# Kernel tuning notes

Hardware: AMD Instinct MI355X
Metric: run time of the kernel (lower is better)

The kernel has to match this reference:

```python
import jax, jax.numpy as jnp
import numpy as np

CHEB_K = 3


def cheb_gcn(x, node_emb, w_pool, b_pool):
    # x: [B, N, C], node_emb: [N, D], w_pool: [D, K, C, O], b_pool: [D, O]
    n = node_emb.shape[0]
    A = jax.nn.softmax(jax.nn.relu(node_emb @ node_emb.T), axis=1)  # [N, N]
    supports = [jnp.eye(n, dtype=x.dtype), A]
    for _ in range(2, CHEB_K):
        supports.append(2.0 * A @ supports[-1] - supports[-2])
    S = jnp.stack(supports, axis=0)  # [K, N, N]
    weights = jnp.einsum('nd,dkio->nkio', node_emb, w_pool)  # [N, K, C, O]
    bias = node_emb @ b_pool  # [N, O]
    x_g = jnp.einsum('knm,bmc->bnkc', S, x)  # [B, N, K, C]
    return jnp.einsum('bnki,nkio->bno', x_g, weights) + bias


def setup_inputs() -> dict:
    key = jax.random.key(0)
    ks = jax.random.split(key, 7)
    B, N, DIN, DOUT, E = 64, 1024, 64, 64, 16
    C = DIN + DOUT
    return {
        'x': jax.random.normal(ks[0], (B, N, DIN), jnp.float32),
        'state': jax.random.normal(ks[1], (B, N, DOUT), jnp.float32),
        'node_embeddings': jax.random.normal(ks[2], (N, E), jnp.float32),
        'W_gate': jax.random.normal(ks[3], (E, CHEB_K, C, 2 * DOUT), jnp.float32) * 0.1,
        'b_gate': jax.random.normal(ks[4], (E, 2 * DOUT), jnp.float32) * 0.1,
        'W_update': jax.random.normal(ks[5], (E, CHEB_K, C, DOUT), jnp.float32) * 0.1,
        'b_update': jax.random.normal(ks[6], (E, DOUT), jnp.float32) * 0.1,
    }


def reference(x, state, node_embeddings, W_gate, b_gate, W_update, b_update):
    hidden = state.shape[-1]
    inp = jnp.concatenate([x, state], axis=-1)  # [B, N, DIN+DOUT]
    z_r = jax.nn.sigmoid(cheb_gcn(inp, node_embeddings, W_gate, b_gate))
    z, r = z_r[..., :hidden], z_r[..., hidden:]
    cand = jnp.concatenate([x, r * state], axis=-1)
    h_hat = jnp.tanh(cheb_gcn(cand, node_embeddings, W_update, b_update))
    return z * state + (1.0 - z) * h_hat
```

## Files before the change

### kernel.cpp

```cpp
#include <hip/hip_runtime.h>
#include <hip/hip_bf16.h>
#include <math.h>

#define B_ 64
#define N_ 1024
#define E_ 16

typedef unsigned short ushort_t;
typedef __attribute__((ext_vector_type(8))) short bf16x8;
typedef __attribute__((ext_vector_type(4))) float f32x4;

__device__ __forceinline__ float sigmoidf_(float x) {
  return 1.0f / (1.0f + __expf(-x));
}
__device__ __forceinline__ ushort_t f2bf(float f) {
  unsigned int u = __float_as_uint(f);
  u = (u + 0x7fffu + ((u >> 16) & 1u)) >> 16;
  return (ushort_t)u;
}
__device__ __forceinline__ float bf2f(ushort_t h) { return __uint_as_float((unsigned)h << 16); }
__device__ __forceinline__ void split_bf(float x, ushort_t& h, ushort_t& l) {
  h = f2bf(x);
  l = f2bf(x - bf2f(h));
}
__device__ __forceinline__ void gload16(const void* g, void* l) {
  __builtin_amdgcn_global_load_lds(
      (const __attribute__((address_space(1))) unsigned int*)g,
      (__attribute__((address_space(3))) unsigned int*)l, 16, 0, 0);
}

__global__ __launch_bounds__(256) void compute_A_kernel(const float* __restrict__ emb,
                                                        ushort_t* __restrict__ Ah,
                                                        ushort_t* __restrict__ Al) {
  __shared__ float embn[E_];
  __shared__ float red[256];
  const int n = blockIdx.x;
  const int t = threadIdx.x;
  if (t < E_) embn[t] = emb[n * E_ + t];
  __syncthreads();
  float s[4];
#pragma unroll
  for (int j = 0; j < 4; ++j) {
    const int m = j * 256 + t;
    const float* em = emb + m * E_;
    float acc = 0.f;
#pragma unroll
    for (int d = 0; d < E_; ++d) acc = fmaf(embn[d], em[d], acc);
    s[j] = fmaxf(acc, 0.f);
  }
  float mx = fmaxf(fmaxf(s[0], s[1]), fmaxf(s[2], s[3]));
  red[t] = mx;
  __syncthreads();
  for (int off = 128; off > 0; off >>= 1) {
    if (t < off) red[t] = fmaxf(red[t], red[t + off]);
    __syncthreads();
  }
  mx = red[0];
  __syncthreads();
  float e[4], lsum = 0.f;
#pragma unroll
  for (int j = 0; j < 4; ++j) { e[j] = __expf(s[j] - mx); lsum += e[j]; }
  red[t] = lsum;
  __syncthreads();
  for (int off = 128; off > 0; off >>= 1) {
    if (t < off) red[t] += red[t + off];
    __syncthreads();
  }
  const float inv = 1.0f / red[0];
#pragma unroll
  for (int j = 0; j < 4; ++j) {
    const float v = e[j] * inv;
    ushort_t h, l;
    split_bf(v, h, l);
    Ah[n * N_ + j * 256 + t] = h;
    Al[n * N_ + j * 256 + t] = l;
  }
}

__global__ __launch_bounds__(256) void build_T0t_kernel(const float* __restrict__ xA,
                                                        const float* __restrict__ xB,
                                                        ushort_t* __restrict__ Th,
                                                        ushort_t* __restrict__ Tl) {
  __shared__ float tile[128][129];
  const int t = threadIdx.x;
  const int b = blockIdx.y;
  const int n0 = blockIdx.x << 7;
  const int c4 = (t & 31) << 2, nl = t >> 5;
#pragma unroll
  for (int p = 0; p < 16; ++p) {
    const int n = nl + (p << 3);
    const float4 v = (c4 < 64)
        ? *(const float4*)&xA[((size_t)b << 16) + ((size_t)(n0 + n) << 6) + c4]
        : *(const float4*)&xB[((size_t)b << 16) + ((size_t)(n0 + n) << 6) + c4 - 64];
    tile[c4 + 0][n] = v.x; tile[c4 + 1][n] = v.y;
    tile[c4 + 2][n] = v.z; tile[c4 + 3][n] = v.w;
  }
  __syncthreads();
  const int c = t >> 1, nc = (t & 1) << 6;
  const size_t obase = ((size_t)(b << 7) + c) * 1024 + n0 + nc;
#pragma unroll
  for (int u = 0; u < 64; u += 4) {
    ushort4 h, l;
    split_bf(tile[c][nc + u + 0], h.x, l.x);
    split_bf(tile[c][nc + u + 1], h.y, l.y);
    split_bf(tile[c][nc + u + 2], h.z, l.z);
    split_bf(tile[c][nc + u + 3], h.w, l.w);
    *(ushort4*)&Th[obase + u] = h;
    *(ushort4*)&Tl[obase + u] = l;
  }
}

template <int PHASE>
__global__ __launch_bounds__(256, 2) void mfma_gemm_kernel(
    const ushort_t* __restrict__ Ah, const ushort_t* __restrict__ Al,
    const ushort_t* __restrict__ Bh, const ushort_t* __restrict__ Bl,
    const ushort_t* __restrict__ T0th, const ushort_t* __restrict__ T0tl,
    float* __restrict__ Yf, ushort_t* __restrict__ Yth, ushort_t* __restrict__ Ytl) {
  __shared__ ushort_t Ah_s[128 * 64], Al_s[128 * 64], Bh_s[128 * 64], Bl_s[128 * 64];
  const int t = threadIdx.x;
  const int wave = t >> 6, lane = t & 63;
  const int n0 = blockIdx.y << 7;
  const int j0 = blockIdx.x << 7;
  const int wr = wave >> 1, wc = wave & 1;
  const int fr = lane & 15, fk = lane >> 4;

  f32x4 acc[4][4];
#pragma unroll
  for (int i = 0; i < 4; ++i)
#pragma unroll
    for (int j = 0; j < 4; ++j) acc[i][j] = (f32x4){0.f, 0.f, 0.f, 0.f};

  const int rsub = lane >> 3;
  const int cp = lane & 7;
  const int selem = (((cp << 4) ^ (rsub << 4)) >> 1);

  for (int k0 = 0; k0 < 1024; k0 += 64) {
    __syncthreads();
#pragma unroll
    for (int i = 0; i < 4; ++i) {
      const int q = (wave << 2) + i;
      const int row = (q << 3) + rsub;
      const int lo = (q << 9) + lane * 8;
      const size_t ga = (size_t)(n0 + row) * 1024 + k0 + selem;
      const size_t gb = (size_t)(j0 + row) * 1024 + k0 + selem;
      gload16(Ah + ga, Ah_s + lo);
      gload16(Al + ga, Al_s + lo);
      gload16(Bh + gb, Bh_s + lo);
      gload16(Bl + gb, Bl_s + lo);
    }
    __syncthreads();
#pragma unroll
    for (int ks = 0; ks < 2; ++ks) {
      bf16x8 ah[4], al[4], bh[4], bl[4];
#pragma unroll
      for (int mi = 0; mi < 4; ++mi) {
        const int r = (wr << 6) + (mi << 4) + fr;
        const int kb = ((ks << 6) + (fk << 4)) ^ ((r & 7) << 4);
        ah[mi] = *(const bf16x8*)((const char*)Ah_s + r * 128 + kb);
        al[mi] = *(const bf16x8*)((const char*)Al_s + r * 128 + kb);
      }
#pragma unroll
      for (int nj = 0; nj < 4; ++nj) {
        const int r = (wc << 6) + (nj << 4) + fr;
        const int kb = ((ks << 6) + (fk << 4)) ^ ((r & 7) << 4);
        bh[nj] = *(const bf16x8*)((const char*)Bh_s + r * 128 + kb);
        bl[nj] = *(const bf16x8*)((const char*)Bl_s + r * 128 + kb);
      }
#pragma unroll
      for (int mi = 0; mi < 4; ++mi)
#pragma unroll
        for (int nj = 0; nj < 4; ++nj) {
          acc[mi][nj] = __builtin_amdgcn_mfma_f32_16x16x32_bf16(ah[mi], bh[nj], acc[mi][nj], 0, 0, 0);
          acc[mi][nj] = __builtin_amdgcn_mfma_f32_16x16x32_bf16(ah[mi], bl[nj], acc[mi][nj], 0, 0, 0);
          acc[mi][nj] = __builtin_amdgcn_mfma_f32_16x16x32_bf16(al[mi], bh[nj], acc[mi][nj], 0, 0, 0);
        }
    }
  }

#pragma unroll
  for (int mi = 0; mi < 4; ++mi) {
    const int nb = n0 + (wr << 6) + (mi << 4) + (fk << 2);
#pragma unroll
    for (int nj = 0; nj < 4; ++nj) {
      const int j = j0 + (wc << 6) + (nj << 4) + fr;
      const f32x4 v = acc[mi][nj];
      if (PHASE == 1) {
#pragma unroll
        for (int r = 0; r < 4; ++r) Yf[(size_t)(nb + r) * 8192 + j] = v[r];
        ushort4 h, l;
        split_bf(v[0], h.x, l.x); split_bf(v[1], h.y, l.y);
        split_bf(v[2], h.z, l.z); split_bf(v[3], h.w, l.w);
        *(ushort4*)&Yth[(size_t)j * 1024 + nb] = h;
        *(ushort4*)&Ytl[(size_t)j * 1024 + nb] = l;
      } else {
        const ushort4 th = *(const ushort4*)&T0th[(size_t)j * 1024 + nb];
        const ushort4 tl = *(const ushort4*)&T0tl[(size_t)j * 1024 + nb];
        float t0r[4];
        t0r[0] = bf2f(th.x) + bf2f(tl.x); t0r[1] = bf2f(th.y) + bf2f(tl.y);
        t0r[2] = bf2f(th.z) + bf2f(tl.z); t0r[3] = bf2f(th.w) + bf2f(tl.w);
#pragma unroll
        for (int r = 0; r < 4; ++r) Yf[(size_t)(nb + r) * 8192 + j] = 2.0f * v[r] - t0r[r];
      }
    }
  }
}

template <int OW_SRC>
__global__ __launch_bounds__(256) void wcombine_half_kernel(const float* __restrict__ emb,
                                                            const float* __restrict__ Wp,
                                                            int o0,
                                                            ushort_t* __restrict__ Wn) {
  __shared__ float es[8][E_];
  const int t = threadIdx.x;
  const int n0 = blockIdx.y * 8;
  if (t < 8 * E_) es[t >> 4][t & 15] = emb[n0 * E_ + t];
  __syncthreads();
  const int j = blockIdx.x * 1024 + t * 4;
  const int k = j >> 13, rem = j & 8191;
  const int i = rem >> 6, o = rem & 63;
  const size_t srcj = (size_t)(k * 128 + i) * OW_SRC + o0 + o;
  const size_t dstr = (size_t)3 * 128 * OW_SRC;
  float4 acc[8] = {};
#pragma unroll 4
  for (int d = 0; d < E_; ++d) {
    const float4 w = *(const float4*)&Wp[d * dstr + srcj];
#pragma unroll
    for (int g = 0; g < 8; ++g) {
      const float e = es[g][d];
      acc[g].x = fmaf(e, w.x, acc[g].x);
      acc[g].y = fmaf(e, w.y, acc[g].y);
      acc[g].z = fmaf(e, w.z, acc[g].z);
      acc[g].w = fmaf(e, w.w, acc[g].w);
    }
  }
#pragma unroll
  for (int g = 0; g < 8; ++g) {
    ushort4 o4;
    o4.x = f2bf(acc[g].x); o4.y = f2bf(acc[g].y);
    o4.z = f2bf(acc[g].z); o4.w = f2bf(acc[g].w);
    *(ushort4*)&Wn[(size_t)(n0 + g) * 24576 + j] = o4;
  }
}

template <int MODE>
__global__ __launch_bounds__(256) void pernode64_kernel(
    const float* __restrict__ xA, const float* __restrict__ xB,
    const float* __restrict__ Y1f, const float* __restrict__ Y2f,
    const ushort_t* __restrict__ Wn,
    const float* __restrict__ emb, const float* __restrict__ bsrc, int bstride,
    const float* __restrict__ state, const float* __restrict__ zb,
    float* __restrict__ dst) {
  __shared__ float XkT[128][68];
  __shared__ float Wf[64][64];
  __shared__ float embn[E_];
  __shared__ float bias[64];
  const int n = blockIdx.x;
  const int t = threadIdx.x;
  if (t < E_) embn[t] = emb[n * E_ + t];
  __syncthreads();
  if (t < 64) {
    float a = 0.f;
#pragma unroll
    for (int d = 0; d < E_; ++d) a = fmaf(embn[d], bsrc[d * bstride + t], a);
    bias[t] = a;
  }
  const int tx = t & 15, ty = t >> 4;
  float acc[4][4] = {};
  const ushort_t* Wb = Wn + (size_t)n * 24576;
#pragma unroll
  for (int k = 0; k < 3; ++k) {
    __syncthreads();
    {
      const int b = t & 63, i0 = (t >> 6) * 32;
      const float* src;
      if (k == 0)
        src = (i0 < 64) ? xA + ((size_t)b << 16) + ((size_t)n << 6) + i0
                        : xB + ((size_t)b << 16) + ((size_t)n << 6) + i0 - 64;
      else if (k == 1)
        src = Y1f + (size_t)n * 8192 + b * 128 + i0;
      else
        src = Y2f + (size_t)n * 8192 + b * 128 + i0;
#pragma unroll
      for (int i = 0; i < 32; ++i) XkT[i0 + i][b] = src[i];
    }
#pragma unroll
    for (int h = 0; h < 2; ++h) {
      if (h) __syncthreads();
      {
        const ushort_t* wsrc = Wb + k * 8192 + h * 4096;
#pragma unroll
        for (int r = 0; r < 2; ++r) {
          const int off = r * 2048 + t * 8;
          const uint4 p = *(const uint4*)&wsrc[off];
          float* dstp = &Wf[0][0] + off;
          dstp[0] = bf2f((ushort_t)(p.x & 0xffff)); dstp[1] = bf2f((ushort_t)(p.x >> 16));
          dstp[2] = bf2f((ushort_t)(p.y & 0xffff)); dstp[3] = bf2f((ushort_t)(p.y >> 16));
          dstp[4] = bf2f((ushort_t)(p.z & 0xffff)); dstp[5] = bf2f((ushort_t)(p.z >> 16));
          dstp[6] = bf2f((ushort_t)(p.w & 0xffff)); dstp[7] = bf2f((ushort_t)(p.w >> 16));
        }
      }
      __syncthreads();
      const int ib = h * 64;
#pragma unroll 4
      for (int ii = 0; ii < 64; ++ii) {
        float xv[4], w[4];
        *(float4*)&xv[0] = *(const float4*)&XkT[ib + ii][ty << 2];
        *(float4*)&w[0] = *(const float4*)&Wf[ii][tx << 2];
#pragma unroll
        for (int bi = 0; bi < 4; ++bi)
#pragma unroll
          for (int oj = 0; oj < 4; ++oj) acc[bi][oj] = fmaf(xv[bi], w[oj], acc[bi][oj]);
      }
    }
  }
#pragma unroll
  for (int bi = 0; bi < 4; ++bi) {
    const int b = (ty << 2) + bi;
    const size_t base = ((size_t)b << 16) + ((size_t)n << 6) + (tx << 2);
    float4 o;
    const float a0 = acc[bi][0] + bias[(tx << 2) + 0];
    const float a1 = acc[bi][1] + bias[(tx << 2) + 1];
    const float a2 = acc[bi][2] + bias[(tx << 2) + 2];
    const float a3 = acc[bi][3] + bias[(tx << 2) + 3];
    if (MODE == 0) {
      o.x = sigmoidf_(a0); o.y = sigmoidf_(a1); o.z = sigmoidf_(a2); o.w = sigmoidf_(a3);
    } else if (MODE == 1) {
      const float4 st = *(const float4*)&state[base];
      o.x = sigmoidf_(a0) * st.x; o.y = sigmoidf_(a1) * st.y;
      o.z = sigmoidf_(a2) * st.z; o.w = sigmoidf_(a3) * st.w;
    } else {
      const float4 st = *(const float4*)&state[base];
      const float4 zv = *(const float4*)&zb[base];
      o.x = zv.x * st.x + (1.f - zv.x) * tanhf(a0);
      o.y = zv.y * st.y + (1.f - zv.y) * tanhf(a1);
      o.z = zv.z * st.z + (1.f - zv.z) * tanhf(a2);
      o.w = zv.w * st.w + (1.f - zv.w) * tanhf(a3);
    }
    *(float4*)&dst[base] = o;
  }
}

extern "C" void kernel_launch(void* const* d_in, const int* in_sizes, int n_in,
                              void* d_out, int out_size, void* d_ws, size_t ws_size,
                              hipStream_t stream) {
  const float* x     = (const float*)d_in[0];
  const float* state = (const float*)d_in[1];
  const float* emb   = (const float*)d_in[2];
  const float* Wg    = (const float*)d_in[3];
  const float* bg    = (const float*)d_in[4];
  const float* Wu    = (const float*)d_in[5];
  const float* bu    = (const float*)d_in[6];
  float* out = (float*)d_out;

  char* w = (char*)d_ws;
  float*    Y1f  = (float*)(w);
  float*    Y2f  = (float*)(w + ((size_t)32 << 20));
  ushort_t* T0th = (ushort_t*)(w + ((size_t)64 << 20));
  ushort_t* T0tl = (ushort_t*)(w + ((size_t)80 << 20));
  ushort_t* Y1th = (ushort_t*)(w + ((size_t)96 << 20));
  ushort_t* Y1tl = (ushort_t*)(w + ((size_t)112 << 20));
  float*    rs   = (float*)(w + ((size_t)128 << 20));
  ushort_t* Ah   = (ushort_t*)(w + ((size_t)144 << 20));
  ushort_t* Al   = (ushort_t*)(w + ((size_t)146 << 20));
  ushort_t* Wn   = (ushort_t*)(w + ((size_t)148 << 20));
  float* zb = out;

  const dim3 gg(64, 8);
  const dim3 gt(8, 64);
  const dim3 gw(24, 128);

  compute_A_kernel<<<N_, 256, 0, stream>>>(emb, Ah, Al);

  build_T0t_kernel<<<gt, 256, 0, stream>>>(x, state, T0th, T0tl);
  mfma_gemm_kernel<1><<<gg, 256, 0, stream>>>(Ah, Al, T0th, T0tl, nullptr, nullptr, Y1f, Y1th, Y1tl);
  mfma_gemm_kernel<0><<<gg, 256, 0, stream>>>(Ah, Al, Y1th, Y1tl, T0th, T0tl, Y2f, nullptr, nullptr);
  wcombine_half_kernel<128><<<gw, 256, 0, stream>>>(emb, Wg, 0, Wn);
  pernode64_kernel<0><<<N_, 256, 0, stream>>>(x, state, Y1f, Y2f, Wn, emb, bg, 128,
                                              nullptr, nullptr, zb);
  wcombine_half_kernel<128><<<gw, 256, 0, stream>>>(emb, Wg, 64, Wn);
  pernode64_kernel<1><<<N_, 256, 0, stream>>>(x, state, Y1f, Y2f, Wn, emb, bg + 64, 128,
                                              state, nullptr, rs);

  build_T0t_kernel<<<gt, 256, 0, stream>>>(x, rs, T0th, T0tl);
  mfma_gemm_kernel<1><<<gg, 256, 0, stream>>>(Ah, Al, T0th, T0tl, nullptr, nullptr, Y1f, Y1th, Y1tl);
  mfma_gemm_kernel<0><<<gg, 256, 0, stream>>>(Ah, Al, Y1th, Y1tl, T0th, T0tl, Y2f, nullptr, nullptr);
  wcombine_half_kernel<64><<<gw, 256, 0, stream>>>(emb, Wu, 0, Wn);
  pernode64_kernel<2><<<N_, 256, 0, stream>>>(x, rs, Y1f, Y2f, Wn, emb, bu, 64,
                                              state, zb, out);
}
```

Measured before the change: 491.2 us.

## Fold T0 subtraction into weights and use MFMA for per-node contraction

The Chebyshev identity S2 = 2A^2 - I is applied by folding the -T0 term into the k=0 weights (W0 - W2). The second GEMM then just scales by 2 and no longer reads T0 in its epilogue. Both GEMMs now write split bf16 hi/lo node-major tiles through LDS instead of fp32 Y buffers. The per-node contraction is rewritten from scalar FP32 FMA to bf16x3 MFMA, with swizzled LDS and async global-to-LDS loads of the pre-transposed weights. This removes the scalar FMA bottleneck and halves the intermediate traffic, at the cost of bf16-split precision in the per-node stage.

```diff
diff --git a/kernel.cpp b/kernel.cpp
--- a/kernel.cpp
+++ b/kernel.cpp
@@ -19,10 +19,6 @@
   return (ushort_t)u;
 }
 __device__ __forceinline__ float bf2f(ushort_t h) { return __uint_as_float((unsigned)h << 16); }
-__device__ __forceinline__ void split_bf(float x, ushort_t& h, ushort_t& l) {
-  h = f2bf(x);
-  l = f2bf(x - bf2f(h));
-}
 __device__ __forceinline__ void gload16(const void* g, void* l) {
   __builtin_amdgcn_global_load_lds(
       (const __attribute__((address_space(1))) unsigned int*)g,
@@ -70,10 +66,9 @@
 #pragma unroll
   for (int j = 0; j < 4; ++j) {
     const float v = e[j] * inv;
-    ushort_t h, l;
-    split_bf(v, h, l);
+    ushort_t h = f2bf(v);
     Ah[n * N_ + j * 256 + t] = h;
-    Al[n * N_ + j * 256 + t] = l;
+    Al[n * N_ + j * 256 + t] = f2bf(v - bf2f(h));
   }
 }
 
@@ -101,10 +96,12 @@
 #pragma unroll
   for (int u = 0; u < 64; u += 4) {
     ushort4 h, l;
-    split_bf(tile[c][nc + u + 0], h.x, l.x);
-    split_bf(tile[c][nc + u + 1], h.y, l.y);
-    split_bf(tile[c][nc + u + 2], h.z, l.z);
-    split_bf(tile[c][nc + u + 3], h.w, l.w);
+    float v0 = tile[c][nc + u + 0], v1 = tile[c][nc + u + 1];
+    float v2 = tile[c][nc + u + 2], v3 = tile[c][nc + u + 3];
+    h.x = f2bf(v0); l.x = f2bf(v0 - bf2f(h.x));
+    h.y = f2bf(v1); l.y = f2bf(v1 - bf2f(h.y));
+    h.z = f2bf(v2); l.z = f2bf(v2 - bf2f(h.z));
+    h.w = f2bf(v3); l.w = f2bf(v3 - bf2f(h.w));
     *(ushort4*)&Th[obase + u] = h;
     *(ushort4*)&Tl[obase + u] = l;
   }
@@ -114,13 +111,18 @@
 __global__ __launch_bounds__(256, 2) void mfma_gemm_kernel(
     const ushort_t* __restrict__ Ah, const ushort_t* __restrict__ Al,
     const ushort_t* __restrict__ Bh, const ushort_t* __restrict__ Bl,
-    const ushort_t* __restrict__ T0th, const ushort_t* __restrict__ T0tl,
-    float* __restrict__ Yf, ushort_t* __restrict__ Yth, ushort_t* __restrict__ Ytl) {
-  __shared__ ushort_t Ah_s[128 * 64], Al_s[128 * 64], Bh_s[128 * 64], Bl_s[128 * 64];
+    ushort_t* __restrict__ Yth, ushort_t* __restrict__ Ytl,
+    ushort_t* __restrict__ XpH, ushort_t* __restrict__ XpL) {
+  __shared__ ushort_t smem[4 * 128 * 64];
+  ushort_t* Ah_s = smem;
+  ushort_t* Al_s = smem + 8192;
+  ushort_t* Bh_s = smem + 16384;
+  ushort_t* Bl_s = smem + 24576;
   const int t = threadIdx.x;
   const int wave = t >> 6, lane = t & 63;
   const int n0 = blockIdx.y << 7;
-  const int j0 = blockIdx.x << 7;
+  const int bcol = blockIdx.x;
+  const int j0 = bcol << 7;
   const int wr = wave >> 1, wc = wave & 1;
   const int fr = lane & 15, fk = lane >> 4;
 
@@ -177,53 +179,72 @@
     }
   }
 
+  __syncthreads();
+  ushort_t* hiT = smem;
+  ushort_t* loT = smem + 16384;
 #pragma unroll
   for (int mi = 0; mi < 4; ++mi) {
-    const int nb = n0 + (wr << 6) + (mi << 4) + (fk << 2);
+    const int nl = (wr << 6) + (mi << 4) + (fk << 2);
 #pragma unroll
     for (int nj = 0; nj < 4; ++nj) {
-      const int j = j0 + (wc << 6) + (nj << 4) + fr;
-      const f32x4 v = acc[mi][nj];
+      const int jl = (wc << 6) + (nj << 4) + fr;
+      const f32x4 vv = acc[mi][nj];
+      ushort_t h[4], l[4];
+#pragma unroll
+      for (int r = 0; r < 4; ++r) {
+        const float v = (PHASE == 1) ? vv[r] : 2.0f * vv[r];
+        h[r] = f2bf(v);
+        l[r] = f2bf(v - bf2f(h[r]));
+      }
       if (PHASE == 1) {
-#pragma unroll
-        for (int r = 0; r < 4; ++r) Yf[(size_t)(nb + r) * 8192 + j] = v[r];
-        ushort4 h, l;
-        split_bf(v[0], h.x, l.x); split_bf(v[1], h.y, l.y);
-        split_bf(v[2], h.z, l.z); split_bf(v[3], h.w, l.w);
-        *(ushort4*)&Yth[(size_t)j * 1024 + nb] = h;
-        *(ushort4*)&Ytl[(size_t)j * 1024 + nb] = l;
-      } else {
-        const ushort4 th = *(const ushort4*)&T0th[(size_t)j * 1024 + nb];
-        const ushort4 tl = *(const ushort4*)&T0tl[(size_t)j * 1024 + nb];
-        float t0r[4];
-        t0r[0] = bf2f(th.x) + bf2f(tl.x); t0r[1] = bf2f(th.y) + bf2f(tl.y);
-        t0r[2] = bf2f(th.z) + bf2f(tl.z); t0r[3] = bf2f(th.w) + bf2f(tl.w);
-#pragma unroll
-        for (int r = 0; r < 4; ++r) Yf[(size_t)(nb + r) * 8192 + j] = 2.0f * v[r] - t0r[r];
-      }
-    }
+        *(ushort4*)&Yth[(size_t)(j0 + jl) * 1024 + n0 + nl] = make_ushort4(h[0], h[1], h[2], h[3]);
+        *(ushort4*)&Ytl[(size_t)(j0 + jl) * 1024 + n0 + nl] = make_ushort4(l[0], l[1], l[2], l[3]);
+      }
+#pragma unroll
+      for (int r = 0; r < 4; ++r) {
+        hiT[(nl + r) * 128 + jl] = h[r];
+        loT[(nl + r) * 128 + jl] = l[r];
+      }
+    }
+  }
+  __syncthreads();
+#pragma unroll
+  for (int rr = 0; rr < 8; ++rr) {
+    const int id = rr * 256 + t;
+    const int nl = id >> 4, ch = id & 15;
+    const size_t dstE = ((size_t)(n0 + nl) * 64 + bcol) * 256 + ch * 8;
+    *(uint4*)&XpH[dstE] = *(const uint4*)((const char*)hiT + nl * 256 + ch * 16);
+    *(uint4*)&XpL[dstE] = *(const uint4*)((const char*)loT + nl * 256 + ch * 16);
   }
 }
 
 template <int OW_SRC>
-__global__ __launch_bounds__(256) void wcombine_half_kernel(const float* __restrict__ emb,
-                                                            const float* __restrict__ Wp,
-                                                            int o0,
-                                                            ushort_t* __restrict__ Wn) {
+__global__ __launch_bounds__(256) void wcombine_t_kernel(const float* __restrict__ emb,
+                                                         const float* __restrict__ Wp,
+                                                         int o0,
+                                                         ushort_t* __restrict__ WtH,
+                                                         ushort_t* __restrict__ WtL) {
   __shared__ float es[8][E_];
+  __shared__ ushort_t tileH[8][8][128];
+  __shared__ ushort_t tileL[8][8][128];
   const int t = threadIdx.x;
   const int n0 = blockIdx.y * 8;
+  const int k  = blockIdx.x >> 3;
+  const int ob = blockIdx.x & 7;
   if (t < 8 * E_) es[t >> 4][t & 15] = emb[n0 * E_ + t];
   __syncthreads();
-  const int j = blockIdx.x * 1024 + t * 4;
-  const int k = j >> 13, rem = j & 8191;
-  const int i = rem >> 6, o = rem & 63;
-  const size_t srcj = (size_t)(k * 128 + i) * OW_SRC + o0 + o;
-  const size_t dstr = (size_t)3 * 128 * OW_SRC;
+  const int i = t >> 1, oq = (t & 1) * 4;
+  const size_t dstr = (size_t)384 * OW_SRC;
+  const size_t src0 = (size_t)(k * 128 + i) * OW_SRC + o0 + ob * 8 + oq;
+  const size_t src2 = (size_t)(2 * 128 + i) * OW_SRC + o0 + ob * 8 + oq;
   float4 acc[8] = {};
 #pragma unroll 4
   for (int d = 0; d < E_; ++d) {
-    const float4 w = *(const float4*)&Wp[d * dstr + srcj];
+    float4 w = *(const float4*)&Wp[d * dstr + src0];
+    if (k == 0) {
+      const float4 w2 = *(const float4*)&Wp[d * dstr + src2];
+      w.x -= w2.x; w.y -= w2.y; w.z -= w2.z; w.w -= w2.w;
+    }
 #pragma unroll
     for (int g = 0; g < 8; ++g) {
       const float e = es[g][d];
@@ -235,23 +256,40 @@
   }
 #pragma unroll
   for (int g = 0; g < 8; ++g) {
-    ushort4 o4;
-    o4.x = f2bf(acc[g].x); o4.y = f2bf(acc[g].y);
-    o4.z = f2bf(acc[g].z); o4.w = f2bf(acc[g].w);
-    *(ushort4*)&Wn[(size_t)(n0 + g) * 24576 + j] = o4;
+    ushort_t h;
+    h = f2bf(acc[g].x); tileH[g][oq + 0][i] = h; tileL[g][oq + 0][i] = f2bf(acc[g].x - bf2f(h));
+    h = f2bf(acc[g].y); tileH[g][oq + 1][i] = h; tileL[g][oq + 1][i] = f2bf(acc[g].y - bf2f(h));
+    h = f2bf(acc[g].z); tileH[g][oq + 2][i] = h; tileL[g][oq + 2][i] = f2bf(acc[g].z - bf2f(h));
+    h = f2bf(acc[g].w); tileH[g][oq + 3][i] = h; tileL[g][oq + 3][i] = f2bf(acc[g].w - bf2f(h));
+  }
+  __syncthreads();
+  const int row = t >> 2, seg = t & 3;
+  const int g = row >> 3, ol = row & 7;
+  const size_t dst = ((size_t)(n0 + g) * 64 + ob * 8 + ol) * 384 + k * 128 + seg * 32;
+  {
+    const uint4* s = (const uint4*)&tileH[g][ol][seg * 32];
+    uint4* dp = (uint4*)&WtH[dst];
+    dp[0] = s[0]; dp[1] = s[1]; dp[2] = s[2]; dp[3] = s[3];
+  }
+  {
+    const uint4* s = (const uint4*)&tileL[g][ol][seg * 32];
+    uint4* dp = (uint4*)&WtL[dst];
+    dp[0] = s[0]; dp[1] = s[1]; dp[2] = s[2]; dp[3] = s[3];
   }
 }
 
 template <int MODE>
-__global__ __launch_bounds__(256) void pernode64_kernel(
+__global__ __launch_bounds__(256, 2) void pernode_mfma_kernel(
     const float* __restrict__ xA, const float* __restrict__ xB,
-    const float* __restrict__ Y1f, const float* __restrict__ Y2f,
-    const ushort_t* __restrict__ Wn,
+    const ushort_t* __restrict__ XpH, const ushort_t* __restrict__ XpL,
+    const ushort_t* __restrict__ WtH, const ushort_t* __restrict__ WtL,
     const float* __restrict__ emb, const float* __restrict__ bsrc, int bstride,
     const float* __restrict__ state, const float* __restrict__ zb,
     float* __restrict__ dst) {
-  __shared__ float XkT[128][68];
-  __shared__ float Wf[64][64];
+  __shared__ ushort_t xh_s[64 * 128];
+  __shared__ ushort_t xl_s[64 * 128];
+  __shared__ ushort_t wh_s[64 * 128];
+  __shared__ ushort_t wl_s[64 * 128];
   __shared__ float embn[E_];
   __shared__ float bias[64];
   const int n = blockIdx.x;
@@ -264,79 +302,103 @@
     for (int d = 0; d < E_; ++d) a = fmaf(embn[d], bsrc[d * bstride + t], a);
     bias[t] = a;
   }
-  const int tx = t & 15, ty = t >> 4;
-  float acc[4][4] = {};
-  const ushort_t* Wb = Wn + (size_t)n * 24576;
-#pragma unroll
-  for (int k = 0; k < 3; ++k) {
-    __syncthreads();
-    {
-      const int b = t & 63, i0 = (t >> 6) * 32;
-      const float* src;
-      if (k == 0)
-        src = (i0 < 64) ? xA + ((size_t)b << 16) + ((size_t)n << 6) + i0
-                        : xB + ((size_t)b << 16) + ((size_t)n << 6) + i0 - 64;
-      else if (k == 1)
-        src = Y1f + (size_t)n * 8192 + b * 128 + i0;
-      else
-        src = Y2f + (size_t)n * 8192 + b * 128 + i0;
-#pragma unroll
-      for (int i = 0; i < 32; ++i) XkT[i0 + i][b] = src[i];
-    }
-#pragma unroll
-    for (int h = 0; h < 2; ++h) {
-      if (h) __syncthreads();
-      {
-        const ushort_t* wsrc = Wb + k * 8192 + h * 4096;
-#pragma unroll
-        for (int r = 0; r < 2; ++r) {
-          const int off = r * 2048 + t * 8;
-          const uint4 p = *(const uint4*)&wsrc[off];
-          float* dstp = &Wf[0][0] + off;
-          dstp[0] = bf2f((ushort_t)(p.x & 0xffff)); dstp[1] = bf2f((ushort_t)(p.x >> 16));
-          dstp[2] = bf2f((ushort_t)(p.y & 0xffff)); dstp[3] = bf2f((ushort_t)(p.y >> 16));
-          dstp[4] = bf2f((ushort_t)(p.z & 0xffff)); dstp[5] = bf2f((ushort_t)(p.z >> 16));
-          dstp[6] = bf2f((ushort_t)(p.w & 0xffff)); dstp[7] = bf2f((ushort_t)(p.w >> 16));
+  const int wave = t >> 6, lane = t & 63;
+  const int fr = lane & 15, fq = lane >> 4;
+  f32x4 acc[4];
+#pragma unroll
+  for (int i = 0; i < 4; ++i) acc[i] = (f32x4){0.f, 0.f, 0.f, 0.f};
+
+#pragma unroll
+  for (int s = 0; s < 3; ++s) {
+    __syncthreads();
+    if (s == 0) {
+      const int b = t >> 2, q = t & 3;
+      const float* srcp = (q < 2)
+          ? xA + ((size_t)b << 16) + ((size_t)n << 6) + (q << 5)
+          : xB + ((size_t)b << 16) + ((size_t)n << 6) + ((q - 2) << 5);
+      float v[32];
+#pragma unroll
+      for (int j = 0; j < 8; ++j) *(float4*)&v[j * 4] = *(const float4*)&srcp[j * 4];
+      const int swz = (b & 7) << 4;
+#pragma unroll
+      for (int jc = 0; jc < 4; ++jc) {
+        unsigned int hh[4], ll[4];
+#pragma unroll
+        for (int e = 0; e < 4; ++e) {
+          const float a0 = v[jc * 8 + 2 * e], a1 = v[jc * 8 + 2 * e + 1];
+          const ushort_t h0 = f2bf(a0), h1 = f2bf(a1);
+          const ushort_t l0 = f2bf(a0 - bf2f(h0)), l1 = f2bf(a1 - bf2f(h1));
+          hh[e] = (unsigned)h0 | ((unsigned)h1 << 16);
+          ll[e] = (unsigned)l0 | ((unsigned)l1 << 16);
         }
-      }
-      __syncthreads();
-      const int ib = h * 64;
-#pragma unroll 4
-      for (int ii = 0; ii < 64; ++ii) {
-        float xv[4], w[4];
-        *(float4*)&xv[0] = *(const float4*)&XkT[ib + ii][ty << 2];
-        *(float4*)&w[0] = *(const float4*)&Wf[ii][tx << 2];
-#pragma unroll
-        for (int bi = 0; bi < 4; ++bi)
-#pragma unroll
-          for (int oj = 0; oj < 4; ++oj) acc[bi][oj] = fmaf(xv[bi], w[oj], acc[bi][oj]);
-      }
-    }
-  }
-#pragma unroll
-  for (int bi = 0; bi < 4; ++bi) {
-    const int b = (ty << 2) + bi;
-    const size_t base = ((size_t)b << 16) + ((size_t)n << 6) + (tx << 2);
-    float4 o;
-    const float a0 = acc[bi][0] + bias[(tx << 2) + 0];
-    const float a1 = acc[bi][1] + bias[(tx << 2) + 1];
-    const float a2 = acc[bi][2] + bias[(tx << 2) + 2];
-    const float a3 = acc[bi][3] + bias[(tx << 2) + 3];
-    if (MODE == 0) {
-      o.x = sigmoidf_(a0); o.y = sigmoidf_(a1); o.z = sigmoidf_(a2); o.w = sigmoidf_(a3);
-    } else if (MODE == 1) {
-      const float4 st = *(const float4*)&state[base];
-      o.x = sigmoidf_(a0) * st.x; o.y = sigmoidf_(a1) * st.y;
-      o.z = sigmoidf_(a2) * st.z; o.w = sigmoidf_(a3) * st.w;
+        const int dstb = b * 256 + (((q << 6) + (jc << 4)) ^ swz);
+        *(uint4*)((char*)xh_s + dstb) = make_uint4(hh[0], hh[1], hh[2], hh[3]);
+        *(uint4*)((char*)xl_s + dstb) = make_uint4(ll[0], ll[1], ll[2], ll[3]);
+      }
     } else {
-      const float4 st = *(const float4*)&state[base];
-      const float4 zv = *(const float4*)&zb[base];
-      o.x = zv.x * st.x + (1.f - zv.x) * tanhf(a0);
-      o.y = zv.y * st.y + (1.f - zv.y) * tanhf(a1);
-      o.z = zv.z * st.z + (1.f - zv.z) * tanhf(a2);
-      o.w = zv.w * st.w + (1.f - zv.w) * tanhf(a3);
-    }
-    *(float4*)&dst[base] = o;
+#pragma unroll
+      for (int r = 0; r < 4; ++r) {
+        const int id = r * 256 + t;
+        const int row = id >> 4, ch = id & 15;
+        const int selem = (((ch << 4) ^ ((row & 7) << 4)) >> 1);
+        const size_t so = ((size_t)n * 64 + row) * 256 + (s - 1) * 128 + selem;
+        gload16(XpH + so, xh_s + id * 8);
+        gload16(XpL + so, xl_s + id * 8);
+      }
+    }
+#pragma unroll
+    for (int r = 0; r < 4; ++r) {
+      const int id = r * 256 + t;
+      const int row = id >> 4, ch = id & 15;
+      const int selem = (((ch << 4) ^ ((row & 7) << 4)) >> 1);
+      const size_t so = ((size_t)n * 64 + row) * 384 + s * 128 + selem;
+      gload16(WtH + so, wh_s + id * 8);
+      gload16(WtL + so, wl_s + id * 8);
+    }
+    __syncthreads();
+#pragma unroll
+    for (int ks = 0; ks < 4; ++ks) {
+      bf16x8 ah[4], al[4];
+#pragma unroll
+      for (int mi = 0; mi < 4; ++mi) {
+        const int r = (mi << 4) + fr;
+        const int kb = ((ks << 6) + (fq << 4)) ^ ((r & 7) << 4);
+        ah[mi] = *(const bf16x8*)((const char*)xh_s + r * 256 + kb);
+        al[mi] = *(const bf16x8*)((const char*)xl_s + r * 256 + kb);
+      }
+      const int rw = (wave << 4) + fr;
+      const int kbw = ((ks << 6) + (fq << 4)) ^ ((rw & 7) << 4);
+      const bf16x8 wh = *(const bf16x8*)((const char*)wh_s + rw * 256 + kbw);
+      const bf16x8 wl = *(const bf16x8*)((const char*)wl_s + rw * 256 + kbw);
+#pragma unroll
+      for (int mi = 0; mi < 4; ++mi) {
+        acc[mi] = __builtin_amdgcn_mfma_f32_16x16x32_bf16(ah[mi], wh, acc[mi], 0, 0, 0);
+        acc[mi] = __builtin_amdgcn_mfma_f32_16x16x32_bf16(al[mi], wh, acc[mi], 0, 0, 0);
+        acc[mi] = __builtin_amdgcn_mfma_f32_16x16x32_bf16(ah[mi], wl, acc[mi], 0, 0, 0);
+      }
+    }
+  }
+
+  const int o = (wave << 4) + fr;
+  const float bia = bias[o];
+#pragma unroll
+  for (int mi = 0; mi < 4; ++mi) {
+    const int b0 = (mi << 4) + (fq << 2);
+    const f32x4 vv = acc[mi];
+#pragma unroll
+    for (int r = 0; r < 4; ++r) {
+      const int b = b0 + r;
+      const size_t base = ((size_t)b << 16) + ((size_t)n << 6);
+      const float a = vv[r] + bia;
+      if (MODE == 0) {
+        dst[base + o] = sigmoidf_(a);
+      } else if (MODE == 1) {
+        dst[base + o] = sigmoidf_(a) * state[base + o];
+      } else {
+        const float z = zb[base + o], st = state[base + o];
+        dst[base + o] = z * st + (1.f - z) * tanhf(a);
+      }
+    }
   }
 }
 
@@ -353,16 +415,17 @@
   float* out = (float*)d_out;
 
   char* w = (char*)d_ws;
-  float*    Y1f  = (float*)(w);
-  float*    Y2f  = (float*)(w + ((size_t)32 << 20));
-  ushort_t* T0th = (ushort_t*)(w + ((size_t)64 << 20));
-  ushort_t* T0tl = (ushort_t*)(w + ((size_t)80 << 20));
-  ushort_t* Y1th = (ushort_t*)(w + ((size_t)96 << 20));
-  ushort_t* Y1tl = (ushort_t*)(w + ((size_t)112 << 20));
-  float*    rs   = (float*)(w + ((size_t)128 << 20));
-  ushort_t* Ah   = (ushort_t*)(w + ((size_t)144 << 20));
-  ushort_t* Al   = (ushort_t*)(w + ((size_t)146 << 20));
-  ushort_t* Wn   = (ushort_t*)(w + ((size_t)148 << 20));
+  ushort_t* Ah   = (ushort_t*)(w);
+  ushort_t* Al   = (ushort_t*)(w + ((size_t)2 << 20));
+  ushort_t* T0th = (ushort_t*)(w + ((size_t)4 << 20));
+  ushort_t* T0tl = (ushort_t*)(w + ((size_t)20 << 20));
+  ushort_t* Y1th = (ushort_t*)(w + ((size_t)36 << 20));
+  ushort_t* Y1tl = (ushort_t*)(w + ((size_t)52 << 20));
+  ushort_t* XpH  = (ushort_t*)(w + ((size_t)68 << 20));
+  ushort_t* XpL  = (ushort_t*)(w + ((size_t)100 << 20));
+  ushort_t* WtH  = (ushort_t*)(w + ((size_t)132 << 20));
+  ushort_t* WtL  = (ushort_t*)(w + ((size_t)180 << 20));
+  float*    rs   = (float*)(w + ((size_t)228 << 20));
   float* zb = out;
 
   const dim3 gg(64, 8);
@@ -370,21 +433,23 @@
   const dim3 gw(24, 128);
 
   compute_A_kernel<<<N_, 256, 0, stream>>>(emb, Ah, Al);
+  wcombine_t_kernel<128><<<gw, 256, 0, stream>>>(emb, Wg, 0, WtH, WtL);
 
   build_T0t_kernel<<<gt, 256, 0, stream>>>(x, state, T0th, T0tl);
-  mfma_gemm_kernel<1><<<gg, 256, 0, stream>>>(Ah, Al, T0th, T0tl, nullptr, nullptr, Y1f, Y1th, Y1tl);
-  mfma_gemm_kernel<0><<<gg, 256, 0, stream>>>(Ah, Al, Y1th, Y1tl, T0th, T0tl, Y2f, nullptr, nullptr);
-  wcombine_half_kernel<128><<<gw, 256, 0, stream>>>(emb, Wg, 0, Wn);
-  pernode64_kernel<0><<<N_, 256, 0, stream>>>(x, state, Y1f, Y2f, Wn, emb, bg, 128,
-                                              nullptr, nullptr, zb);
-  wcombine_half_kernel<128><<<gw, 256, 0, stream>>>(emb, Wg, 64, Wn);
-  pernode64_kernel<1><<<N_, 256, 0, stream>>>(x, state, Y1f, Y2f, Wn, emb, bg + 64, 128,
-                                              state, nullptr, rs);
-
+  mfma_gemm_kernel<1><<<gg, 256, 0, stream>>>(Ah, Al, T0th, T0tl, Y1th, Y1tl, XpH, XpL);
+  mfma_gemm_kernel<0><<<gg, 256, 0, stream>>>(Ah, Al, Y1th, Y1tl, nullptr, nullptr,
+                                              XpH + 128, XpL + 128);
+  pernode_mfma_kernel<0><<<N_, 256, 0, stream>>>(x, state, XpH, XpL, WtH, WtL, emb, bg, 128,
+                                                 state, nullptr, zb);
+  wcombine_t_kernel<128><<<gw, 256, 0, stream>>>(emb, Wg, 64, WtH, WtL);
+  pernode_mfma_kernel<1><<<N_, 256, 0, stream>>>(x, state, XpH, XpL, WtH, WtL, emb, bg + 64, 128,
+                                                 state, nullptr, rs);
+
+  wcombine_t_kernel<64><<<gw, 256, 0, stream>>>(emb, Wu, 0, WtH, WtL);
   build_T0t_kernel<<<gt, 256, 0, stream>>>(x, rs, T0th, T0tl);
-  mfma_gemm_kernel<1><<<gg, 256, 0, stream>>>(Ah, Al, T0th, T0tl, nullptr, nullptr, Y1f, Y1th, Y1tl);
-  mfma_gemm_kernel<0><<<gg, 256, 0, stream>>>(Ah, Al, Y1th, Y1tl, T0th, T0tl, Y2f, nullptr, nullptr);
-  wcombine_half_kernel<64><<<gw, 256, 0, stream>>>(emb, Wu, 0, Wn);
-  pernode64_kernel<2><<<N_, 256, 0, stream>>>(x, rs, Y1f, Y2f, Wn, emb, bu, 64,
-                                              state, zb, out);
-}
+  mfma_gemm_kernel<1><<<gg, 256, 0, stream>>>(Ah, Al, T0th, T0tl, Y1th, Y1tl, XpH, XpL);
+  mfma_gemm_kernel<0><<<gg, 256, 0, stream>>>(Ah, Al, Y1th, Y1tl, nullptr, nullptr,
+                                              XpH + 128, XpL + 128);
+  pernode_mfma_kernel<2><<<N_, 256, 0, stream>>>(x, rs, XpH, XpL, WtH, WtL, emb, bu, 64,
+                                                 state, zb, out);
+}
```

Result: slower. 569.6 us (+16.0%).
